# Kernel optimization log

Measured on AMD Instinct MI355X. Metric: run time of the kernel, lower is better.

The kernel has to match this reference:

```python
import jax, jax.numpy as jnp
import numpy as np

BETA = 1.0  # init_kwargs beta

B, D, N = 8, 3, 4096
LATENT = 256

def setup_inputs() -> dict:
    key = jax.random.key(0)
    k1, k2, k3, k4 = jax.random.split(key, 4)
    return {
        "recon_x": jax.random.normal(k1, (B, D, N), dtype=jnp.float32),
        "x": jax.random.normal(k2, (B, D, N), dtype=jnp.float32),
        "mu": jax.random.normal(k3, (B, LATENT), dtype=jnp.float32),
        "logvar": jax.random.normal(k4, (B, LATENT), dtype=jnp.float32),
    }

def _chamfer(xc, yc):
    # xc, yc: [B, D, N] channels-first point clouds -> [B, N, D]
    xp = jnp.swapaxes(xc, 2, 1)  # [B, N, D]
    yp = jnp.swapaxes(yc, 2, 1)  # [B, M, D]
    # squared L2 pairwise distances via gram expansion (avoids [B,N,M,D] intermediate)
    x2 = jnp.sum(xp * xp, axis=-1)               # [B, N]
    y2 = jnp.sum(yp * yp, axis=-1)               # [B, M]
    xy = jnp.einsum("bnd,bmd->bnm", xp, yp)      # [B, N, M]
    dist = x2[:, :, None] + y2[:, None, :] - 2.0 * xy  # [B, N, M]
    min_x = jnp.min(dist, axis=2)  # [B, N] nearest y for each x
    min_y = jnp.min(dist, axis=1)  # [B, M] nearest x for each y
    return jnp.mean(min_x) + jnp.mean(min_y)

def _kl(mu, logvar):
    kld = -0.5 * jnp.sum(1.0 + logvar - mu * mu - jnp.exp(logvar))
    return kld / mu.shape[0]

def reference(recon_x, x, mu, logvar):
    recon_loss = _chamfer(recon_x, x)
    kld_loss = _kl(mu, logvar)
    total_loss = recon_loss + BETA * kld_loss
    return (total_loss, recon_loss, kld_loss)
```

## Files before the change

### kernel.cpp

```cpp
#include <hip/hip_runtime.h>
#include <math.h>

#define BB 8
#define NN 4096
#define LATENT 256

#define THREADS 256
#define Q 4
#define QB (Q * THREADS)
#define QTILES (NN / QB)
#define BLOCKS_X (2 * BB * QTILES)
#define CSPLIT 32
#define TT (NN / CSPLIT)
#define NSLOTS (2 * BB * NN)

__device__ __forceinline__ unsigned enc(float f) {
    unsigned b = __float_as_uint(f);
    return (b & 0x80000000u) ? ~b : (b | 0x80000000u);
}
__device__ __forceinline__ float dec(unsigned k) {
    unsigned b = (k & 0x80000000u) ? (k ^ 0x80000000u) : ~k;
    return __uint_as_float(b);
}

__global__ __launch_bounds__(THREADS, 6)
void chamfer_stage1(const float* __restrict__ recon,
                    const float* __restrict__ x,
                    unsigned* __restrict__ minkeys,
                    unsigned* __restrict__ counter)
{
    __shared__ float4 ly[TT];

    const int bx  = blockIdx.x;
    const int c   = blockIdx.y;
    const int dir = bx >> 5;
    const int rem = bx & 31;
    const int b   = rem >> 2;
    const int qt  = rem & 3;
    const int tid = threadIdx.x;

    if (bx == 0 && c == 0 && tid == 0) *counter = 0u;

    const float* cloud = (dir ? recon : x) + (size_t)b * 3 * NN;
    const float* query = (dir ? x : recon) + (size_t)b * 3 * NN;

    for (int i = tid; i < TT; i += THREADS) {
        int m = c * TT + i;
        float y0 = cloud[m];
        float y1 = cloud[NN + m];
        float y2 = cloud[2 * NN + m];
        ly[i] = make_float4(-2.0f * y0, -2.0f * y1, -2.0f * y2,
                            y0 * y0 + y1 * y1 + y2 * y2);
    }
    __syncthreads();

    const int q0 = qt * QB + tid;
    float px[Q], py[Q], pz[Q], mn[Q];
#pragma unroll
    for (int k = 0; k < Q; ++k) {
        int q = q0 + k * THREADS;
        px[k] = query[q];
        py[k] = query[NN + q];
        pz[k] = query[2 * NN + q];
        mn[k] = 3.4e38f;
    }

    float4 va = ly[0], vb = ly[1];
#pragma unroll 4
    for (int m = 0; m < TT - 2; m += 2) {
        float4 na = ly[m + 2];
        float4 nb = ly[m + 3];
#pragma unroll
        for (int k = 0; k < Q; ++k) {
            float t0 = fmaf(px[k], va.x, fmaf(py[k], va.y, fmaf(pz[k], va.z, va.w)));
            float t1 = fmaf(px[k], vb.x, fmaf(py[k], vb.y, fmaf(pz[k], vb.z, vb.w)));
            mn[k] = fminf(fminf(mn[k], t0), t1);
        }
        va = na; vb = nb;
    }
#pragma unroll
    for (int k = 0; k < Q; ++k) {
        float t0 = fmaf(px[k], va.x, fmaf(py[k], va.y, fmaf(pz[k], va.z, va.w)));
        float t1 = fmaf(px[k], vb.x, fmaf(py[k], vb.y, fmaf(pz[k], vb.z, vb.w)));
        mn[k] = fminf(fminf(mn[k], t0), t1);
        float sx  = fmaf(px[k], px[k], fmaf(py[k], py[k], pz[k] * pz[k]));
        float val = sx + mn[k];
        int slot  = dir * (BB * NN) + b * NN + q0 + k * THREADS;
        atomicMin(&minkeys[slot], enc(val));
    }
}

__global__ __launch_bounds__(THREADS)
void chamfer_stage2(const unsigned* __restrict__ minkeys,
                    const float* __restrict__ mu,
                    const float* __restrict__ logvar,
                    float* __restrict__ sums,
                    unsigned* __restrict__ counter,
                    float* __restrict__ out)
{
    __shared__ float red[4];
    __shared__ float redA[4];
    __shared__ float redB[4];
    __shared__ int amLast;

    const int tid = threadIdx.x;
    const int bid = blockIdx.x;

    float v = dec(minkeys[bid * THREADS + tid]);
    for (int off = 32; off > 0; off >>= 1)
        v += __shfl_down(v, off);
    if ((tid & 63) == 0) red[tid >> 6] = v;
    __syncthreads();

    if (tid == 0) {
        float tot = red[0] + red[1] + red[2] + red[3];
        __hip_atomic_store(&sums[bid], tot, __ATOMIC_RELEASE, __HIP_MEMORY_SCOPE_AGENT);
        unsigned old = __hip_atomic_fetch_add(counter, 1u, __ATOMIC_ACQ_REL, __HIP_MEMORY_SCOPE_AGENT);
        amLast = (old == 255u);
    }
    __syncthreads();
    if (!amLast) return;

    float s = __hip_atomic_load(&sums[tid], __ATOMIC_ACQUIRE, __HIP_MEMORY_SCOPE_AGENT);

    float kl = 0.0f;
    for (int i = tid; i < BB * LATENT; i += THREADS) {
        float m  = mu[i];
        float lv = logvar[i];
        kl += 1.0f + lv - m * m - expf(lv);
    }

    for (int off = 32; off > 0; off >>= 1) {
        s  += __shfl_down(s, off);
        kl += __shfl_down(kl, off);
    }
    if ((tid & 63) == 0) { redA[tid >> 6] = s; redB[tid >> 6] = kl; }
    __syncthreads();
    if (tid == 0) {
        float recon = (redA[0] + redA[1] + redA[2] + redA[3]) / (float)(BB * NN);
        float kld   = -0.5f * (redB[0] + redB[1] + redB[2] + redB[3]) / (float)BB;
        out[0] = recon + kld;
        out[1] = recon;
        out[2] = kld;
    }
}

extern "C" void kernel_launch(void* const* d_in, const int* in_sizes, int n_in,
                              void* d_out, int out_size, void* d_ws, size_t ws_size,
                              hipStream_t stream)
{
    const float* recon  = (const float*)d_in[0];
    const float* x      = (const float*)d_in[1];
    const float* mu     = (const float*)d_in[2];
    const float* logvar = (const float*)d_in[3];
    float* out = (float*)d_out;

    unsigned* minkeys = (unsigned*)d_ws;
    float*    sums    = (float*)(minkeys + NSLOTS);
    unsigned* counter = (unsigned*)(sums + 256);

    hipMemsetAsync(minkeys, 0xFF, (size_t)NSLOTS * sizeof(unsigned), stream);

    dim3 g1(BLOCKS_X, CSPLIT);
    chamfer_stage1<<<g1, THREADS, 0, stream>>>(recon, x, minkeys, counter);
    chamfer_stage2<<<NSLOTS / THREADS, THREADS, 0, stream>>>(minkeys, mu, logvar,
                                                             sums, counter, out);
}
```

Before: 41.28 us.

## Use packed FP32 FMA and min3 with 16 queries per thread in chamfer

Each thread now handles 16 query points, packed as pairs into float2 registers. Distances are computed with inline-asm v_pk_fma_f32 using op_sel to broadcast the cloud components, and the running minimum uses v_min3_f32. The grid is reshaped so each block covers all queries for one (dir,batch) against a 64-way split of the cloud, which means more atomics per slot. The memset is replaced by an init kernel that also resets the counter. The aim is to double FMA throughput through packed math and cut min instructions, at the cost of higher register pressure and lower occupancy.

```diff
diff --git a/kernel.cpp b/kernel.cpp
--- a/kernel.cpp
+++ b/kernel.cpp
@@ -6,13 +6,11 @@
 #define LATENT 256
 
 #define THREADS 256
-#define Q 4
-#define QB (Q * THREADS)
-#define QTILES (NN / QB)
-#define BLOCKS_X (2 * BB * QTILES)
-#define CSPLIT 32
+#define P 8
+#define CSPLIT 64
 #define TT (NN / CSPLIT)
 #define NSLOTS (2 * BB * NN)
+#define BLOCKS_X (2 * BB)
 
 __device__ __forceinline__ unsigned enc(float f) {
     unsigned b = __float_as_uint(f);
@@ -23,70 +21,95 @@
     return __uint_as_float(b);
 }
 
-__global__ __launch_bounds__(THREADS, 6)
+__device__ __forceinline__ float min3f(float a, float b, float c) {
+    float d;
+    asm("v_min3_f32 %0, %1, %2, %3" : "=v"(d) : "v"(a), "v"(b), "v"(c));
+    return d;
+}
+
+__device__ __forceinline__ float2 dist_pk(float2 cxy, float2 czw,
+                                          float2 qx, float2 qy, float2 qz) {
+    float2 t;
+    asm("v_pk_fma_f32 %0, %1, %2, %1 op_sel:[0,0,1] op_sel_hi:[0,1,1]"
+        : "=v"(t) : "v"(czw), "v"(qz));
+    asm("v_pk_fma_f32 %0, %1, %2, %0 op_sel:[1,0,0] op_sel_hi:[1,1,1]"
+        : "+v"(t) : "v"(cxy), "v"(qy));
+    asm("v_pk_fma_f32 %0, %1, %2, %0 op_sel:[0,0,0] op_sel_hi:[0,1,1]"
+        : "+v"(t) : "v"(cxy), "v"(qx));
+    return t;
+}
+
+__global__ __launch_bounds__(THREADS)
+void init_kernel(unsigned* __restrict__ minkeys, unsigned* __restrict__ counter)
+{
+    int i = blockIdx.x * THREADS + threadIdx.x;
+    minkeys[i] = 0xFFFFFFFFu;
+    if (i == 0) *counter = 0u;
+}
+
+__global__ __launch_bounds__(THREADS, 4)
 void chamfer_stage1(const float* __restrict__ recon,
                     const float* __restrict__ x,
-                    unsigned* __restrict__ minkeys,
-                    unsigned* __restrict__ counter)
+                    unsigned* __restrict__ minkeys)
 {
     __shared__ float4 ly[TT];
 
     const int bx  = blockIdx.x;
     const int c   = blockIdx.y;
-    const int dir = bx >> 5;
-    const int rem = bx & 31;
-    const int b   = rem >> 2;
-    const int qt  = rem & 3;
+    const int dir = bx >> 3;
+    const int b   = bx & 7;
     const int tid = threadIdx.x;
-
-    if (bx == 0 && c == 0 && tid == 0) *counter = 0u;
 
     const float* cloud = (dir ? recon : x) + (size_t)b * 3 * NN;
     const float* query = (dir ? x : recon) + (size_t)b * 3 * NN;
 
-    for (int i = tid; i < TT; i += THREADS) {
-        int m = c * TT + i;
+    if (tid < TT) {
+        int m = c * TT + tid;
         float y0 = cloud[m];
         float y1 = cloud[NN + m];
         float y2 = cloud[2 * NN + m];
-        ly[i] = make_float4(-2.0f * y0, -2.0f * y1, -2.0f * y2,
-                            y0 * y0 + y1 * y1 + y2 * y2);
+        ly[tid] = make_float4(-2.0f * y0, -2.0f * y1, -2.0f * y2,
+                              y0 * y0 + y1 * y1 + y2 * y2);
     }
     __syncthreads();
 
-    const int q0 = qt * QB + tid;
-    float px[Q], py[Q], pz[Q], mn[Q];
+    float2 qx[P], qy[P], qz[P];
+    float mn0[P], mn1[P];
 #pragma unroll
-    for (int k = 0; k < Q; ++k) {
-        int q = q0 + k * THREADS;
-        px[k] = query[q];
-        py[k] = query[NN + q];
-        pz[k] = query[2 * NN + q];
-        mn[k] = 3.4e38f;
+    for (int p = 0; p < P; ++p) {
+        int ql = p * THREADS + tid;
+        int qh = ql + 2048;
+        qx[p] = make_float2(query[ql],          query[qh]);
+        qy[p] = make_float2(query[NN + ql],     query[NN + qh]);
+        qz[p] = make_float2(query[2 * NN + ql], query[2 * NN + qh]);
+        mn0[p] = 3.4e38f;
+        mn1[p] = 3.4e38f;
     }
 
-    float4 va = ly[0], vb = ly[1];
 #pragma unroll 4
-    for (int m = 0; m < TT - 2; m += 2) {
-        float4 na = ly[m + 2];
-        float4 nb = ly[m + 3];
+    for (int j = 0; j < TT; j += 2) {
+        float4 A = ly[j];
+        float4 B = ly[j + 1];
+        float2 Axy = make_float2(A.x, A.y), Azw = make_float2(A.z, A.w);
+        float2 Bxy = make_float2(B.x, B.y), Bzw = make_float2(B.z, B.w);
 #pragma unroll
-        for (int k = 0; k < Q; ++k) {
-            float t0 = fmaf(px[k], va.x, fmaf(py[k], va.y, fmaf(pz[k], va.z, va.w)));
-            float t1 = fmaf(px[k], vb.x, fmaf(py[k], vb.y, fmaf(pz[k], vb.z, vb.w)));
-            mn[k] = fminf(fminf(mn[k], t0), t1);
+        for (int p = 0; p < P; ++p) {
+            float2 ta = dist_pk(Axy, Azw, qx[p], qy[p], qz[p]);
+            float2 tb = dist_pk(Bxy, Bzw, qx[p], qy[p], qz[p]);
+            mn0[p] = min3f(mn0[p], ta.x, tb.x);
+            mn1[p] = min3f(mn1[p], ta.y, tb.y);
         }
-        va = na; vb = nb;
     }
+
+    const int base = dir * (BB * NN) + b * NN;
 #pragma unroll
-    for (int k = 0; k < Q; ++k) {
-        float t0 = fmaf(px[k], va.x, fmaf(py[k], va.y, fmaf(pz[k], va.z, va.w)));
-        float t1 = fmaf(px[k], vb.x, fmaf(py[k], vb.y, fmaf(pz[k], vb.z, vb.w)));
-        mn[k] = fminf(fminf(mn[k], t0), t1);
-        float sx  = fmaf(px[k], px[k], fmaf(py[k], py[k], pz[k] * pz[k]));
-        float val = sx + mn[k];
-        int slot  = dir * (BB * NN) + b * NN + q0 + k * THREADS;
-        atomicMin(&minkeys[slot], enc(val));
+    for (int p = 0; p < P; ++p) {
+        int ql = p * THREADS + tid;
+        int qh = ql + 2048;
+        float sx0 = fmaf(qx[p].x, qx[p].x, fmaf(qy[p].x, qy[p].x, qz[p].x * qz[p].x));
+        float sx1 = fmaf(qx[p].y, qx[p].y, fmaf(qy[p].y, qy[p].y, qz[p].y * qz[p].y));
+        atomicMin(&minkeys[base + ql], enc(sx0 + mn0[p]));
+        atomicMin(&minkeys[base + qh], enc(sx1 + mn1[p]));
     }
 }
 
@@ -159,10 +182,11 @@
     float*    sums    = (float*)(minkeys + NSLOTS);
     unsigned* counter = (unsigned*)(sums + 256);
 
-    hipMemsetAsync(minkeys, 0xFF, (size_t)NSLOTS * sizeof(unsigned), stream);
+    init_kernel<<<NSLOTS / THREADS, THREADS, 0, stream>>>(minkeys, counter);
 
     dim3 g1(BLOCKS_X, CSPLIT);
-    chamfer_stage1<<<g1, THREADS, 0, stream>>>(recon, x, minkeys, counter);
+    chamfer_stage1<<<g1, THREADS, 0, stream>>>(recon, x, minkeys);
+
     chamfer_stage2<<<NSLOTS / THREADS, THREADS, 0, stream>>>(minkeys, mu, logvar,
                                                              sums, counter, out);
 }
```

Result: slower. 43.77 us (+6.0%).
